# Performance work log

Measured on AMD Instinct MI355X. Metric: run time of the kernel, lower is better.

Reference implementation:

```python
import jax, jax.numpy as jnp
import numpy as np
from jax import lax

N = 16384; B = 8; L = N // B; E = 262144
UNI = 496; PE = 16; C = UNI + PE   # channels = 512 (num_heads_gnn=1 so hidden*heads == hidden)
S = 16; K = 4; DTR = 32            # mamba d_state=16, d_conv=4, dt_rank=ceil(512/16)=32


def _sinpe(pos, d):
    # matches sinusoidal_positional_embedding: emb[:,0::2]=sin(pos/denom), emb[:,1::2]=cos
    half = d // 2
    denom = jnp.power(10000.0, 2.0 * jnp.arange(half, dtype=pos.dtype) / d)
    ang = pos[:, None] / denom                       # [N, d//2]
    return jnp.stack([jnp.sin(ang), jnp.cos(ang)], axis=-1).reshape(pos.shape[0], d)


def _bn(h, g, b, eps=1e-5):
    # BatchNorm1d over node dim, batch statistics (training-style)
    mu = h.mean(0)
    var = jnp.mean((h - mu) ** 2, axis=0)
    return (h - mu) * lax.rsqrt(var + eps) * g + b


def setup_inputs() -> dict:
    key = jax.random.key(0)
    ks = jax.random.split(key, 48)
    r = lambda i, shape, s=0.02: jax.random.normal(ks[i], shape, jnp.float32) * s
    src = jax.random.randint(ks[0], (E,), 0, N, jnp.int32)
    off = jax.random.randint(ks[1], (E,), 1, N, jnp.int32)
    dst = (src + off) % N  # no self-loops: GATConv strips then re-adds them
    return dict(
        x=jax.random.normal(ks[2], (N, 1026), jnp.float32),
        edge_index=jnp.stack([src, dst]),
        edge_cat=jax.random.randint(ks[4], (E,), 0, 21, jnp.int32),
        edge_cont=jax.random.normal(ks[3], (E, 2), jnp.float32),
        batch=(jnp.arange(N, dtype=jnp.int32) // L),  # B contiguous equal-size graphs
        W_uni=r(5, (1024, UNI), 0.03), b_uni=r(6, (UNI,)),
        edge_emb=r(7, (21, 16), 1.0), W_edge=r(8, (2, 16), 0.5), b_edge=r(9, (16,)),
        W_gat=r(10, (C, C), 0.04), att_src=r(11, (C,), 0.06), att_dst=r(12, (C,), 0.06), b_gat=r(13, (C,)),
        g1=jnp.ones((C,), jnp.float32), be1=jnp.zeros((C,), jnp.float32),
        g2=jnp.ones((C,), jnp.float32), be2=jnp.zeros((C,), jnp.float32),
        g3=jnp.ones((C,), jnp.float32), be3=jnp.zeros((C,), jnp.float32),
        W_in=r(14, (C, 2 * C), 0.04), w_conv=r(15, (C, K), 0.3), b_conv=r(16, (C,)),
        W_xp=r(17, (C, DTR + 2 * S), 0.04), W_dt=r(18, (DTR, C), 0.1), b_dt=r(19, (C,), 0.5),
        A_log=jnp.log(jnp.tile(jnp.arange(1, S + 1, dtype=jnp.float32)[None, :], (C, 1))),
        D_p=jnp.ones((C,), jnp.float32), W_out=r(20, (C, C), 0.04),
        W_m1=r(21, (C, 2 * C), 0.04), b_m1=r(22, (2 * C,)),
        W_m2=r(23, (2 * C, C), 0.03), b_m2=r(24, (C,)),
        Wf1=r(25, (C, C // 2), 0.04), bf1=r(26, (C // 2,)),
        Wf2=r(27, (C // 2, C // 4), 0.06), bf2=r(28, (C // 4,)),
        Wf3=r(29, (C // 4, 1), 0.1), bf3=r(30, (1,)),
    )


def _forward(x, edge_cont, W_uni, b_uni, edge_emb, W_edge, b_edge, W_gat, att_src, att_dst,
             b_gat, g1, be1, g2, be2, g3, be3, W_in, w_conv, b_conv, W_xp, W_dt, b_dt,
             A_log, D_p, W_out, W_m1, b_m1, W_m2, b_m2, Wf1, bf1, Wf2, bf2, Wf3, bf3,
             edge_index, edge_cat, batch):
    # --- node features: UNI projection + 2D sinusoidal PE ---
    pe = jnp.concatenate([_sinpe(x[:, 0], PE // 2), _sinpe(x[:, 1], PE // 2)], axis=-1)  # [N,16]
    xf = x[:, 2:2 + 1024] @ W_uni + b_uni                                                # [N,496]
    h0 = jnp.concatenate([xf, pe], axis=-1)                                              # [N,512]
    # edge features are computed as in the original, but GATConv(edge_dim=None) ignores them
    _ef = edge_emb[edge_cat] + edge_cont @ W_edge + b_edge

    # --- GATConv, heads=1, concat, with self loops, eval (no dropout) ---
    xh = h0 @ W_gat                                  # [N,C]
    a_s = xh @ att_src                               # [N]
    a_d = xh @ att_dst
    loops = jnp.arange(N)
    src = jnp.concatenate([edge_index[0], loops])
    dst = jnp.concatenate([edge_index[1], loops])
    alpha = jax.nn.leaky_relu(a_s[src] + a_d[dst], 0.2)
    amax = jax.ops.segment_max(alpha, dst, num_segments=N)
    ea = jnp.exp(alpha - amax[dst])
    den = jax.ops.segment_sum(ea, dst, num_segments=N)
    w = ea / (den[dst] + 1e-16)
    gat = jax.ops.segment_sum(w[:, None] * xh[src], dst, num_segments=N) + b_gat
    h1 = _bn(gat, g1, be1)

    # --- Mamba branch on the LAYER INPUT h0; equal contiguous graphs -> reshape ---
    hd = h0.reshape(B, L, C)
    xz = hd @ W_in                                   # [B,L,2C]
    xm, z = xz[..., :C], xz[..., C:]
    xp = jnp.pad(xm, ((0, 0), (K - 1, 0), (0, 0)))   # causal depthwise conv, kernel K
    xc = b_conv + sum(xp[:, k:k + L, :] * w_conv[:, k] for k in range(K))
    xc = jax.nn.silu(xc)
    proj = xc @ W_xp                                 # [B,L,DTR+2S]
    dt = jax.nn.softplus(proj[..., :DTR] @ W_dt + b_dt)   # [B,L,C]
    Bm = proj[..., DTR:DTR + S]
    Cm = proj[..., DTR + S:]
    A = -jnp.exp(A_log)                              # [C,S]

    def step(hst, inp):
        xt, dtt, Bt, Ct = inp                        # [B,C],[B,C],[B,S],[B,S]
        hst = hst * jnp.exp(dtt[:, :, None] * A) + (dtt * xt)[:, :, None] * Bt[:, None, :]
        return hst, jnp.einsum('bds,bs->bd', hst, Ct)

    _, ys = lax.scan(step, jnp.zeros((B, C, S), hd.dtype),
                     (xc.swapaxes(0, 1), dt.swapaxes(0, 1), Bm.swapaxes(0, 1), Cm.swapaxes(0, 1)))
    y = ys.swapaxes(0, 1) + D_p * xc
    y = (y * jax.nn.silu(z)) @ W_out                 # [B,L,C]
    h2 = _bn(y.reshape(N, C), g2, be2)

    # --- combine, MLP residual, norm3, relu ---
    out = h1 + h2
    out = out + (jax.nn.relu(out @ W_m1 + b_m1) @ W_m2 + b_m2)
    out = jax.nn.relu(_bn(out, g3, be3))

    # --- global mean pool + head MLP ---
    pooled = out.reshape(B, L, C).mean(axis=1)       # [B,C]
    hm = jax.nn.relu(pooled @ Wf1 + bf1)
    hm = jax.nn.relu(hm @ Wf2 + bf2)
    pred = hm @ Wf3 + bf3                            # [B,1]
    return pred, pooled


def reference(x, edge_index, edge_cat, edge_cont, batch, W_uni, b_uni, edge_emb, W_edge,
              b_edge, W_gat, att_src, att_dst, b_gat, g1, be1, g2, be2, g3, be3, W_in,
              w_conv, b_conv, W_xp, W_dt, b_dt, A_log, D_p, W_out, W_m1, b_m1, W_m2, b_m2,
              Wf1, bf1, Wf2, bf2, Wf3, bf3):
    return _forward(x, edge_cont, W_uni, b_uni, edge_emb, W_edge, b_edge, W_gat, att_src,
                    att_dst, b_gat, g1, be1, g2, be2, g3, be3, W_in, w_conv, b_conv, W_xp,
                    W_dt, b_dt, A_log, D_p, W_out, W_m1, b_m1, W_m2, b_m2, Wf1, bf1, Wf2,
                    bf2, Wf3, bf3, edge_index, edge_cat, batch)
```

## Files before the change

### kernel.cpp

```cpp
#include <hip/hip_runtime.h>
#include <math.h>

#define NN 16384
#define CD 512
#define EE 262144
#define LL 2048
#define NCK 32
#define TC 64

typedef __attribute__((ext_vector_type(8))) short short8;
typedef __attribute__((ext_vector_type(4))) float floatx4;

__device__ __forceinline__ unsigned short f2b(float f){
  unsigned int u = __float_as_uint(f);
  unsigned int r = (u + 0x7fffu + ((u>>16)&1u)) >> 16;
  return (unsigned short)r;
}
__device__ __forceinline__ float b2f(unsigned short h){
  return __uint_as_float(((unsigned int)h)<<16);
}


__global__ void transposeW(const float* __restrict__ W, short* __restrict__ Bt,
                           int K, int Nsub, int Npad, int pitch, int col0){
  int idx = blockIdx.x*256 + threadIdx.x;
  if (idx >= Npad*K) return;
  int n = idx / K, k = idx - n*K;
  float v = (n < Nsub) ? W[(size_t)k*pitch + col0 + n] : 0.f;
  Bt[idx] = (short)f2b(v);
}

__global__ void fuse_wdt(const float* __restrict__ W_xp, const float* __restrict__ W_dt,
                         short* __restrict__ Wft){
  int idx = blockIdx.x*256 + threadIdx.x;
  if (idx >= 512*512) return;
  int i = idx & 511;
  int j = idx >> 9;
  float a = 0.f;
  #pragma unroll 8
  for (int r = 0; r < 32; ++r) a += W_xp[(size_t)i*64 + r] * W_dt[(size_t)r*512 + j];
  Wft[idx] = (short)f2b(a);
}

__global__ void pad_bias(const float* __restrict__ b, float* __restrict__ out){
  int i = blockIdx.x*256 + threadIdx.x;
  if (i < 512) out[i] = (i < 496) ? b[i] : 0.f;
}

__global__ void conv_x(const float* __restrict__ x, short* __restrict__ Xb){
  int idx = blockIdx.x*256 + threadIdx.x;
  if (idx >= NN*1024) return;
  int r = idx >> 10, c = idx & 1023;
  Xb[idx] = (short)f2b(x[(size_t)r*1026 + 2 + c]);
}

__global__ void pe_fill(const float* __restrict__ x, unsigned short* __restrict__ h0b){
  int r = blockIdx.x*256 + threadIdx.x;
  if (r >= NN) return;
  float p0 = x[(size_t)r*1026 + 0], p1 = x[(size_t)r*1026 + 1];
  const float dn[4] = {1.f, 10.f, 100.f, 1000.f};
  unsigned short* o = h0b + (size_t)r*512 + 496;
  #pragma unroll
  for (int q = 0; q < 4; ++q){
    o[2*q]     = f2b(sinf(p0/dn[q]));
    o[2*q+1]   = f2b(cosf(p0/dn[q]));
    o[8+2*q]   = f2b(sinf(p1/dn[q]));
    o[8+2*q+1] = f2b(cosf(p1/dn[q]));
  }
}

#define GLDS(g, l) __builtin_amdgcn_global_load_lds((const __attribute__((address_space(1))) void*)(g), (__attribute__((address_space(3))) void*)(l), 16, 0, 0)

__global__ __launch_bounds__(256)
void gemm_bt(const short* __restrict__ A, const short* __restrict__ Bt,
             float* __restrict__ Cf, unsigned short* __restrict__ Cb,
             const float* __restrict__ bias, const float* __restrict__ resid,
             int K, int Nvalid, int epi){
  __shared__ __align__(16) short As[128*32];
  __shared__ __align__(16) short Bs[128*32];
  int tid = threadIdx.x;
  int m0 = blockIdx.x * 128;
  int n0 = blockIdx.y * 128;
  int lane = tid & 63, wave = tid >> 6;
  int wm = wave >> 1, wn = wave & 1;
  int lr = lane & 15, lk = lane >> 4;

  floatx4 acc[4][4];
  #pragma unroll
  for (int m = 0; m < 4; ++m)
    #pragma unroll
    for (int n = 0; n < 4; ++n) acc[m][n] = (floatx4)0.f;

  int wrow = wave * 32;
  int srow = lane >> 2;
  int scol = (lane & 3) * 8;

  const short* gA0 = A  + (size_t)(m0 + wrow + srow)*K      + scol;
  const short* gA1 = A  + (size_t)(m0 + wrow + 16 + srow)*K + scol;
  const short* gB0 = Bt + (size_t)(n0 + wrow + srow)*K      + scol;
  const short* gB1 = Bt + (size_t)(n0 + wrow + 16 + srow)*K + scol;

  for (int k0 = 0; k0 < K; k0 += 32){
    __syncthreads();
    GLDS(gA0 + k0, &As[wrow*32]);
    GLDS(gA1 + k0, &As[(wrow+16)*32]);
    GLDS(gB0 + k0, &Bs[wrow*32]);
    GLDS(gB1 + k0, &Bs[(wrow+16)*32]);
    __syncthreads();
    short8 af[4], bf[4];
    #pragma unroll
    for (int m = 0; m < 4; ++m) af[m] = *(const short8*)&As[(wm*64 + m*16 + lr)*32 + lk*8];
    #pragma unroll
    for (int n = 0; n < 4; ++n) bf[n] = *(const short8*)&Bs[(wn*64 + n*16 + lr)*32 + lk*8];
    #pragma unroll
    for (int m = 0; m < 4; ++m)
      #pragma unroll
      for (int n = 0; n < 4; ++n)
        acc[m][n] = __builtin_amdgcn_mfma_f32_16x16x32_bf16(af[m], bf[n], acc[m][n], 0, 0, 0);
  }

  #pragma unroll
  for (int m = 0; m < 4; ++m){
    #pragma unroll
    for (int n = 0; n < 4; ++n){
      int col = n0 + wn*64 + n*16 + lr;
      if (col < Nvalid){
        #pragma unroll
        for (int r = 0; r < 4; ++r){
          int row = m0 + wm*64 + m*16 + lk*4 + r;
          float v = acc[m][n][r];
          if (bias)  v += bias[col];
          if (resid) v += resid[(size_t)row*Nvalid + col];
          if (epi == 1) v = fmaxf(v, 0.f);
          else if (epi == 2) v = (v > 20.f) ? v : log1pf(expf(v));
          size_t o = (size_t)row*Nvalid + col;
          if (Cf) Cf[o] = v;
          if (Cb) Cb[o] = f2b(v);
        }
      }
    }
  }
}

__global__ void att_proj(const unsigned short* __restrict__ xh,
                         const float* __restrict__ att_src, const float* __restrict__ att_dst,
                         float* __restrict__ a_s, float* __restrict__ a_d){
  int wave = threadIdx.x >> 6, lane = threadIdx.x & 63;
  int r = blockIdx.x*4 + wave;
  const unsigned short* xr = xh + (size_t)r*512;
  float ps = 0.f, pd = 0.f;
  #pragma unroll
  for (int j = 0; j < 8; ++j){
    float v = b2f(xr[lane + 64*j]);
    ps += v * att_src[lane + 64*j];
    pd += v * att_dst[lane + 64*j];
  }
  #pragma unroll
  for (int m = 32; m >= 1; m >>= 1){ ps += __shfl_xor(ps, m); pd += __shfl_xor(pd, m); }
  if (lane == 0){ a_s[r] = ps; a_d[r] = pd; }
}

__global__ void gat_hist(const int* __restrict__ ei, int* __restrict__ cnt){
  int e = blockIdx.x*256 + threadIdx.x;
  if (e < EE) atomicAdd(&cnt[ei[EE + e]], 1);
}

__global__ void gat_prefix(const int* __restrict__ cnt, int* __restrict__ offsets, int* __restrict__ cursor){
  __shared__ int part[256];
  int t = threadIdx.x;
  int s = 0;
  for (int i = 0; i < 64; ++i) s += cnt[t*64 + i];
  part[t] = s;
  __syncthreads();
  for (int off = 1; off < 256; off <<= 1){
    int v = (t >= off) ? part[t - off] : 0;
    __syncthreads();
    part[t] += v;
    __syncthreads();
  }
  int run = part[t] - s;
  for (int i = 0; i < 64; ++i){
    int c = cnt[t*64 + i];
    offsets[t*64 + i] = run;
    cursor[t*64 + i]  = run;
    run += c;
  }
  if (t == 255) offsets[NN] = run;
}

__global__ void gat_scatter(const int* __restrict__ ei, const float* __restrict__ a_s,
                            const float* __restrict__ a_d, int* __restrict__ cursor,
                            int* __restrict__ srcs, float* __restrict__ alphas){
  int e = blockIdx.x*256 + threadIdx.x;
  if (e >= EE) return;
  int sN = ei[e], dN = ei[EE + e];
  int p = atomicAdd(&cursor[dN], 1);
  srcs[p] = sN;
  float al = a_s[sN] + a_d[dN];
  alphas[p] = (al > 0.f) ? al : 0.2f*al;
}

__global__ __launch_bounds__(256)
void gat_agg(const int* __restrict__ offsets, const int* __restrict__ srcs,
             const float* __restrict__ alphas, const unsigned short* __restrict__ xh,
             const float* __restrict__ a_s, const float* __restrict__ a_d,
             const float* __restrict__ b_gat, float* __restrict__ gat){
  int wave = threadIdx.x >> 6, lane = threadIdx.x & 63;
  int i = blockIdx.x*4 + wave;
  int beg = offsets[i], end = offsets[i+1];
  float asd = a_s[i] + a_d[i];
  float al0 = (asd > 0.f) ? asd : 0.2f*asd;
  float mx = al0;
  for (int p = beg + lane; p < end; p += 64) mx = fmaxf(mx, alphas[p]);
  #pragma unroll
  for (int m = 32; m >= 1; m >>= 1) mx = fmaxf(mx, __shfl_xor(mx, m));
  float se = 0.f;
  for (int p = beg + lane; p < end; p += 64) se += expf(alphas[p] - mx);
  #pragma unroll
  for (int m = 32; m >= 1; m >>= 1) se += __shfl_xor(se, m);
  float den = se + expf(al0 - mx);
  float inv = 1.f/(den + 1e-16f);
  float acc[8] = {0,0,0,0,0,0,0,0};
  for (int p = beg; p < end; ++p){
    float w = expf(alphas[p] - mx) * inv;
    const unsigned short* xr = xh + (size_t)srcs[p]*512;
    #pragma unroll
    for (int j = 0; j < 8; ++j) acc[j] += w * b2f(xr[lane + 64*j]);
  }
  {
    float w0 = expf(al0 - mx) * inv;
    const unsigned short* xr = xh + (size_t)i*512;
    #pragma unroll
    for (int j = 0; j < 8; ++j) acc[j] += w0 * b2f(xr[lane + 64*j]);
  }
  #pragma unroll
  for (int j = 0; j < 8; ++j)
    gat[(size_t)i*512 + lane + 64*j] = acc[j] + b_gat[lane + 64*j];
}

__global__ void conv_silu(const unsigned short* __restrict__ xzb,
                          const float* __restrict__ w_conv, const float* __restrict__ b_conv,
                          float* __restrict__ xc, unsigned short* __restrict__ xcb){
  int r = blockIdx.x;
  int c = blockIdx.y*256 + threadIdx.x;
  int t = r & (LL - 1);
  float acc = b_conv[c];
  #pragma unroll
  for (int k = 0; k < 4; ++k){
    int tt = t + k - 3;
    if (tt >= 0) acc += b2f(xzb[(size_t)(r + k - 3)*1024 + c]) * w_conv[c*4 + k];
  }
  float s = acc / (1.f + expf(-acc));
  xc[(size_t)r*512 + c] = s;
  xcb[(size_t)r*512 + c] = f2b(s);
}

__global__ __launch_bounds__(256)
void ssm_scan1(const float* __restrict__ dt, const float* __restrict__ xc,
               const float* __restrict__ BC, const float* __restrict__ A_log,
               float* __restrict__ Pc, float* __restrict__ Hc){
  int s  = threadIdx.x & 15;
  int dl = threadIdx.x >> 4;
  int bc = blockIdx.x;
  int b  = bc >> 5;
  int ck = bc & (NCK - 1);
  int d  = blockIdx.y*16 + dl;
  float A = -expf(A_log[d*16 + s]);
  float h = 0.f, P = 1.f;
  size_t r = (size_t)b*LL + (size_t)ck*TC;
  for (int t = 0; t < TC; ++t, ++r){
    float dtv = dt[r*512 + d];
    float xv  = xc[r*512 + d];
    float Bv  = BC[r*32 + s];
    float a = expf(dtv * A);
    h = h*a + (dtv*xv)*Bv;
    P *= a;
  }
  size_t idx = ((size_t)bc*512 + d)*16 + s;
  Pc[idx] = P;
  Hc[idx] = h;
}

__global__ void ssm_carry(const float* __restrict__ Pc, float* __restrict__ Hc){
  int gid = blockIdx.x*256 + threadIdx.x;
  int b  = gid >> 13;
  int ds = gid & 8191;
  size_t idx = ((size_t)b*NCK)*8192 + ds;
  float carry = 0.f;
  for (int c = 0; c < NCK; ++c){
    float P = Pc[idx], H = Hc[idx];
    Hc[idx] = carry;
    carry = H + P*carry;
    idx += 8192;
  }
}

__global__ __launch_bounds__(256)
void ssm_scan2(const float* __restrict__ dt, const float* __restrict__ xc,
               const float* __restrict__ BC, const unsigned short* __restrict__ xzb,
               const float* __restrict__ A_log, const float* __restrict__ D_p,
               const float* __restrict__ Cin, unsigned short* __restrict__ yfb){
  int s  = threadIdx.x & 15;
  int dl = threadIdx.x >> 4;
  int bc = blockIdx.x;
  int b  = bc >> 5;
  int ck = bc & (NCK - 1);
  int d  = blockIdx.y*16 + dl;
  float A = -expf(A_log[d*16 + s]);
  float Dp = D_p[d];
  size_t idx = ((size_t)bc*512 + d)*16 + s;
  float h = Cin[idx];
  size_t r = (size_t)b*LL + (size_t)ck*TC;
  for (int t = 0; t < TC; ++t, ++r){
    float dtv = dt[r*512 + d];
    float xv  = xc[r*512 + d];
    float Bv  = BC[r*32 + s];
    float Cv  = BC[r*32 + 16 + s];
    float a = expf(dtv * A);
    h = h*a + (dtv*xv)*Bv;
    float y = h * Cv;
    y += __shfl_xor(y, 1);
    y += __shfl_xor(y, 2);
    y += __shfl_xor(y, 4);
    y += __shfl_xor(y, 8);
    if (s == 0){
      float z  = b2f(xzb[r*1024 + 512 + d]);
      float sz = z / (1.f + expf(-z));
      yfb[r*512 + d] = f2b((y + Dp*xv) * sz);
    }
  }
}

__global__ void colstats(const float* __restrict__ X, float* __restrict__ sums, float* __restrict__ sqs){
  int c0 = threadIdx.x;
  int row0 = blockIdx.x * 128;
  float s0=0,q0=0,s1=0,q1=0;
  for (int i = 0; i < 128; ++i){
    const float* rp = X + (size_t)(row0+i)*512;
    float a = rp[c0], b = rp[c0+256];
    s0 += a; q0 += a*a; s1 += b; q1 += b*b;
  }
  atomicAdd(&sums[c0], s0);      atomicAdd(&sqs[c0], q0);
  atomicAdd(&sums[c0+256], s1);  atomicAdd(&sqs[c0+256], q1);
}

__global__ void combine_out0(const float* __restrict__ gat, const float* __restrict__ h2,
                             const float* __restrict__ s1, const float* __restrict__ q1,
                             const float* __restrict__ s2, const float* __restrict__ q2,
                             const float* __restrict__ g1, const float* __restrict__ be1,
                             const float* __restrict__ g2, const float* __restrict__ be2,
                             float* __restrict__ out0, unsigned short* __restrict__ out0b){
  int t = threadIdx.x;
  int row0 = blockIdx.x * 128;
  const float invN = 1.f/16384.f;
  float sc1[2], sc2[2], off[2];
  #pragma unroll
  for (int h = 0; h < 2; ++h){
    int c = t + h*256;
    float m1 = s1[c]*invN, v1 = q1[c]*invN - m1*m1;
    float m2 = s2[c]*invN, v2 = q2[c]*invN - m2*m2;
    float a1 = rsqrtf(v1 + 1e-5f) * g1[c];
    float a2 = rsqrtf(v2 + 1e-5f) * g2[c];
    sc1[h] = a1; sc2[h] = a2;
    off[h] = be1[c] + be2[c] - m1*a1 - m2*a2;
  }
  for (int i = 0; i < 128; ++i){
    size_t ro = (size_t)(row0+i)*512;
    #pragma unroll
    for (int h = 0; h < 2; ++h){
      int c = t + h*256;
      float v = gat[ro+c]*sc1[h] + h2[ro+c]*sc2[h] + off[h];
      out0[ro+c] = v;
      out0b[ro+c] = f2b(v);
    }
  }
}

__global__ void out2_pool(const float* __restrict__ out1,
                          const float* __restrict__ s3, const float* __restrict__ q3,
                          const float* __restrict__ g3, const float* __restrict__ be3,
                          float* __restrict__ poolsum){
  int t = threadIdx.x;
  int row0 = blockIdx.x * 128;
  int bidx = row0 / LL;
  const float invN = 1.f/16384.f;
  float sc[2], off[2], acc[2] = {0.f, 0.f};
  #pragma unroll
  for (int h = 0; h < 2; ++h){
    int c = t + h*256;
    float m = s3[c]*invN, v = q3[c]*invN - m*m;
    float a = rsqrtf(v + 1e-5f) * g3[c];
    sc[h] = a; off[h] = be3[c] - m*a;
  }
  for (int i = 0; i < 128; ++i){
    size_t ro = (size_t)(row0+i)*512;
    #pragma unroll
    for (int h = 0; h < 2; ++h){
      int c = t + h*256;
      float v = fmaxf(out1[ro+c]*sc[h] + off[h], 0.f);
      acc[h] += v;
    }
  }
  atomicAdd(&poolsum[bidx*512 + t], acc[0]);
  atomicAdd(&poolsum[bidx*512 + t + 256], acc[1]);
}

__global__ __launch_bounds__(256)
void head(const float* __restrict__ poolsum,
          const float* __restrict__ Wf1, const float* __restrict__ bf1,
          const float* __restrict__ Wf2, const float* __restrict__ bf2,
          const float* __restrict__ Wf3, const float* __restrict__ bf3,
          float* __restrict__ dout){
  int r = blockIdx.x, t = threadIdx.x;
  __shared__ float pool[512];
  __shared__ float h1s[256];
  __shared__ float h2s[128];
  for (int i = t; i < 512; i += 256){
    float v = poolsum[r*512 + i] * (1.f/2048.f);
    pool[i] = v;
    dout[8 + r*512 + i] = v;
  }
  __syncthreads();
  {
    float a = bf1[t];
    for (int k = 0; k < 512; ++k) a += pool[k] * Wf1[(size_t)k*256 + t];
    h1s[t] = fmaxf(a, 0.f);
  }
  __syncthreads();
  if (t < 128){
    float a = bf2[t];
    for (int k = 0; k < 256; ++k) a += h1s[k] * Wf2[(size_t)k*128 + t];
    h2s[t] = fmaxf(a, 0.f);
  }
  __syncthreads();
  if (t == 0){
    float a = bf3[0];
    for (int k = 0; k < 128; ++k) a += h2s[k] * Wf3[k];
    dout[r] = a;
  }
}

extern "C" void kernel_launch(void* const* d_in, const int* in_sizes, int n_in,
                              void* d_out, int out_size, void* d_ws, size_t ws_size,
                              hipStream_t stream){
  const float* x      = (const float*)d_in[0];
  const int*   ei     = (const int*)d_in[1];
  const float* W_uni  = (const float*)d_in[5];
  const float* b_uni  = (const float*)d_in[6];
  const float* W_gat  = (const float*)d_in[10];
  const float* att_s  = (const float*)d_in[11];
  const float* att_d  = (const float*)d_in[12];
  const float* b_gat  = (const float*)d_in[13];
  const float* g1     = (const float*)d_in[14];
  const float* be1    = (const float*)d_in[15];
  const float* g2     = (const float*)d_in[16];
  const float* be2    = (const float*)d_in[17];
  const float* g3     = (const float*)d_in[18];
  const float* be3    = (const float*)d_in[19];
  const float* W_in   = (const float*)d_in[20];
  const float* w_conv = (const float*)d_in[21];
  const float* b_conv = (const float*)d_in[22];
  const float* W_xp   = (const float*)d_in[23];
  const float* W_dt   = (const float*)d_in[24];
  const float* b_dt   = (const float*)d_in[25];
  const float* A_log  = (const float*)d_in[26];
  const float* D_p    = (const float*)d_in[27];
  const float* W_out  = (const float*)d_in[28];
  const float* W_m1   = (const float*)d_in[29];
  const float* b_m1   = (const float*)d_in[30];
  const float* W_m2   = (const float*)d_in[31];
  const float* b_m2   = (const float*)d_in[32];
  const float* Wf1    = (const float*)d_in[33];
  const float* bf1    = (const float*)d_in[34];
  const float* Wf2    = (const float*)d_in[35];
  const float* bf2    = (const float*)d_in[36];
  const float* Wf3    = (const float*)d_in[37];
  const float* bf3    = (const float*)d_in[38];
  float* dout = (float*)d_out;

  char* base = (char*)d_ws;
  size_t off = 0;
  auto alloc = [&](size_t b){ size_t r = off; off += (b + 255) & ~(size_t)255; return r; };

  size_t oR1    = alloc((size_t)NN*1024*2);
  size_t oH0b   = alloc((size_t)NN*512*2);
  size_t oWuniT = alloc(512*1024*2);
  size_t oWgatT = alloc(512*512*2);
  size_t oWinT  = alloc(1024*512*2);
  size_t oWfusT = alloc(512*512*2);
  size_t oWbcT  = alloc(128*512*2);
  size_t oWoutT = alloc(512*512*2);
  size_t oWm1T  = alloc(1024*512*2);
  size_t oWm2T  = alloc(512*1024*2);
  size_t oBuni  = alloc(512*4);
  size_t oXh    = alloc((size_t)NN*512*2);
  size_t oAs    = alloc(NN*4);
  size_t oAd    = alloc(NN*4);
  size_t oCnt   = alloc(NN*4);
  size_t oCur   = alloc(NN*4);
  size_t oOff   = alloc((NN+1)*4);
  size_t oSrcs  = alloc((size_t)EE*4);
  size_t oAlph  = alloc((size_t)EE*4);
  size_t oGat   = alloc((size_t)NN*512*4);
  size_t oXc    = alloc((size_t)NN*512*4);
  size_t oXcb   = alloc((size_t)NN*512*2);
  size_t oDt    = alloc((size_t)NN*512*4);
  size_t oBC    = alloc((size_t)NN*32*4);
  size_t oStats = alloc(6*512*4);
  size_t oPool  = alloc(8*512*4);

  short* Xb   = (short*)(base + oR1);
  unsigned short* xzb = (unsigned short*)(base + oR1);
  float* out1 = (float*)(base + oR1);
  unsigned short* h0b = (unsigned short*)(base + oH0b);
  short* WuniT = (short*)(base + oWuniT);
  short* WgatT = (short*)(base + oWgatT);
  short* WinT  = (short*)(base + oWinT);
  short* WfusT = (short*)(base + oWfusT);
  short* WbcT  = (short*)(base + oWbcT);
  short* WoutT = (short*)(base + oWoutT);
  short* Wm1T  = (short*)(base + oWm1T);
  short* Wm2T  = (short*)(base + oWm2T);
  float* buniP = (float*)(base + oBuni);
  unsigned short* xh  = (unsigned short*)(base + oXh);
  unsigned short* yfb = (unsigned short*)(base + oXh);
  float* a_s = (float*)(base + oAs);
  float* a_d = (float*)(base + oAd);
  int* cnt = (int*)(base + oCnt);
  int* cur = (int*)(base + oCur);
  int* offs = (int*)(base + oOff);
  int* srcs = (int*)(base + oSrcs);
  float* alphas = (float*)(base + oAlph);
  float* gat = (float*)(base + oGat);
  unsigned short* mlp1b = (unsigned short*)(base + oGat);
  float* xc = (float*)(base + oXc);
  float* out0 = (float*)(base + oXc);
  unsigned short* xcb  = (unsigned short*)(base + oXcb);
  unsigned short* out0b = (unsigned short*)(base + oXcb);
  float* Pc = (float*)(base + oXcb);
  float* Hc = Pc + (size_t)8*NCK*512*16;
  float* dt = (float*)(base + oDt);
  float* h2raw = (float*)(base + oDt);
  float* BC = (float*)(base + oBC);
  float* s1 = (float*)(base + oStats);
  float* q1 = s1 + 512;
  float* s2 = q1 + 512;
  float* q2 = s2 + 512;
  float* s3 = q2 + 512;
  float* q3 = s3 + 512;
  float* poolsum = (float*)(base + oPool);

  hipMemsetAsync(cnt, 0, NN*4, stream);
  hipMemsetAsync(s1, 0, 6*512*4, stream);
  hipMemsetAsync(poolsum, 0, 8*512*4, stream);

  transposeW<<<(512*1024+255)/256, 256, 0, stream>>>(W_uni, WuniT, 1024, 496, 512, 496, 0);
  transposeW<<<(512*512+255)/256, 256, 0, stream>>>(W_gat, WgatT, 512, 512, 512, 512, 0);
  transposeW<<<(1024*512+255)/256, 256, 0, stream>>>(W_in, WinT, 512, 1024, 1024, 1024, 0);
  transposeW<<<(128*512+255)/256, 256, 0, stream>>>(W_xp, WbcT, 512, 32, 128, 64, 32);
  transposeW<<<(512*512+255)/256, 256, 0, stream>>>(W_out, WoutT, 512, 512, 512, 512, 0);
  transposeW<<<(1024*512+255)/256, 256, 0, stream>>>(W_m1, Wm1T, 512, 1024, 1024, 1024, 0);
  transposeW<<<(512*1024+255)/256, 256, 0, stream>>>(W_m2, Wm2T, 1024, 512, 512, 512, 0);
  fuse_wdt<<<(512*512+255)/256, 256, 0, stream>>>(W_xp, W_dt, WfusT);
  pad_bias<<<2, 256, 0, stream>>>(b_uni, buniP);
  conv_x<<<(NN*1024+255)/256, 256, 0, stream>>>(x, Xb);

  dim3 g4(128, 4), g8(128, 8), g1b(128, 1);
  gemm_bt<<<g4, 256, 0, stream>>>(Xb, WuniT, nullptr, h0b, buniP, nullptr, 1024, 512, 0);
  pe_fill<<<(NN+255)/256, 256, 0, stream>>>(x, h0b);
  gemm_bt<<<g4, 256, 0, stream>>>((const short*)h0b, WgatT, nullptr, xh, nullptr, nullptr, 512, 512, 0);
  att_proj<<<NN/4, 256, 0, stream>>>(xh, att_s, att_d, a_s, a_d);
  gat_hist<<<EE/256, 256, 0, stream>>>(ei, cnt);
  gat_prefix<<<1, 256, 0, stream>>>(cnt, offs, cur);
  gat_scatter<<<EE/256, 256, 0, stream>>>(ei, a_s, a_d, cur, srcs, alphas);
  gat_agg<<<NN/4, 256, 0, stream>>>(offs, srcs, alphas, xh, a_s, a_d, b_gat, gat);
  colstats<<<128, 256, 0, stream>>>(gat, s1, q1);
  gemm_bt<<<g8, 256, 0, stream>>>((const short*)h0b, WinT, nullptr, xzb, nullptr, nullptr, 512, 1024, 0);
  {
    dim3 gc(NN, 2);
    conv_silu<<<gc, 256, 0, stream>>>(xzb, w_conv, b_conv, xc, xcb);
  }
  gemm_bt<<<g4, 256, 0, stream>>>((const short*)xcb, WfusT, dt, nullptr, b_dt, nullptr, 512, 512, 2);
  gemm_bt<<<g1b, 256, 0, stream>>>((const short*)xcb, WbcT, BC, nullptr, nullptr, nullptr, 512, 32, 0);
  {
    dim3 gs(8*NCK, 32);
    ssm_scan1<<<gs, 256, 0, stream>>>(dt, xc, BC, A_log, Pc, Hc);
    ssm_carry<<<256, 256, 0, stream>>>(Pc, Hc);
    ssm_scan2<<<gs, 256, 0, stream>>>(dt, xc, BC, xzb, A_log, D_p, Hc, yfb);
  }
  gemm_bt<<<g4, 256, 0, stream>>>((const short*)yfb, WoutT, h2raw, nullptr, nullptr, nullptr, 512, 512, 0);
  colstats<<<128, 256, 0, stream>>>(h2raw, s2, q2);
  combine_out0<<<128, 256, 0, stream>>>(gat, h2raw, s1, q1, s2, q2, g1, be1, g2, be2, out0, out0b);
  gemm_bt<<<g8, 256, 0, stream>>>((const short*)out0b, Wm1T, nullptr, mlp1b, b_m1, nullptr, 512, 1024, 1);
  gemm_bt<<<g4, 256, 0, stream>>>((const short*)mlp1b, Wm2T, out1, nullptr, b_m2, out0, 1024, 512, 0);
  colstats<<<128, 256, 0, stream>>>(out1, s3, q3);
  out2_pool<<<128, 256, 0, stream>>>(out1, s3, q3, g3, be3, poolsum);
  head<<<8, 256, 0, stream>>>(poolsum, Wf1, bf1, Wf2, bf2, Wf3, bf3, dout);
}
```

Measured before the change: 1.117 ms.

## Restructure SSM scan to one thread per channel holding all 16 states

The selective-scan kernels now give each thread one channel and keep all 16 state values in registers, instead of one thread per (channel, state) pair. dt and x are loaded once per channel rather than 16 times, B and C are read as vector loads, and the cross-lane shuffle reduction for y is removed. The chunk decay product is computed in closed form as exp(A·sum(dt)). Fast __expf replaces expf in the GAT aggregation, conv SiLU and scan kernels. The scan grids shrink from 32 to 2 y-blocks, which lowers parallelism and raises register pressure, and the fast exp and closed-form product may change rounding slightly.

Measured after the change: 915.2 us. -18.1%, faster.

```diff
diff --git a/kernel.cpp b/kernel.cpp
--- a/kernel.cpp
+++ b/kernel.cpp
@@ -215,20 +215,20 @@
   #pragma unroll
   for (int m = 32; m >= 1; m >>= 1) mx = fmaxf(mx, __shfl_xor(mx, m));
   float se = 0.f;
-  for (int p = beg + lane; p < end; p += 64) se += expf(alphas[p] - mx);
+  for (int p = beg + lane; p < end; p += 64) se += __expf(alphas[p] - mx);
   #pragma unroll
   for (int m = 32; m >= 1; m >>= 1) se += __shfl_xor(se, m);
-  float den = se + expf(al0 - mx);
+  float den = se + __expf(al0 - mx);
   float inv = 1.f/(den + 1e-16f);
   float acc[8] = {0,0,0,0,0,0,0,0};
   for (int p = beg; p < end; ++p){
-    float w = expf(alphas[p] - mx) * inv;
+    float w = __expf(alphas[p] - mx) * inv;
     const unsigned short* xr = xh + (size_t)srcs[p]*512;
     #pragma unroll
     for (int j = 0; j < 8; ++j) acc[j] += w * b2f(xr[lane + 64*j]);
   }
   {
-    float w0 = expf(al0 - mx) * inv;
+    float w0 = __expf(al0 - mx) * inv;
     const unsigned short* xr = xh + (size_t)i*512;
     #pragma unroll
     for (int j = 0; j < 8; ++j) acc[j] += w0 * b2f(xr[lane + 64*j]);
@@ -250,7 +250,7 @@
     int tt = t + k - 3;
     if (tt >= 0) acc += b2f(xzb[(size_t)(r + k - 3)*1024 + c]) * w_conv[c*4 + k];
   }
-  float s = acc / (1.f + expf(-acc));
+  float s = acc / (1.f + __expf(-acc));
   xc[(size_t)r*512 + c] = s;
   xcb[(size_t)r*512 + c] = f2b(s);
 }
@@ -259,26 +259,41 @@
 void ssm_scan1(const float* __restrict__ dt, const float* __restrict__ xc,
                const float* __restrict__ BC, const float* __restrict__ A_log,
                float* __restrict__ Pc, float* __restrict__ Hc){
-  int s  = threadIdx.x & 15;
-  int dl = threadIdx.x >> 4;
+  int d  = blockIdx.y*256 + threadIdx.x;
   int bc = blockIdx.x;
   int b  = bc >> 5;
   int ck = bc & (NCK - 1);
-  int d  = blockIdx.y*16 + dl;
-  float A = -expf(A_log[d*16 + s]);
-  float h = 0.f, P = 1.f;
+  float A[16], h[16];
+  #pragma unroll
+  for (int s = 0; s < 16; ++s){ A[s] = -__expf(A_log[d*16 + s]); h[s] = 0.f; }
+  float sdt = 0.f;
   size_t r = (size_t)b*LL + (size_t)ck*TC;
   for (int t = 0; t < TC; ++t, ++r){
     float dtv = dt[r*512 + d];
     float xv  = xc[r*512 + d];
-    float Bv  = BC[r*32 + s];
-    float a = expf(dtv * A);
-    h = h*a + (dtv*xv)*Bv;
-    P *= a;
-  }
-  size_t idx = ((size_t)bc*512 + d)*16 + s;
-  Pc[idx] = P;
-  Hc[idx] = h;
+    float dx  = dtv * xv;
+    const floatx4* bp = (const floatx4*)&BC[r*32];
+    float Bf[16];
+    *(floatx4*)&Bf[0]  = bp[0];
+    *(floatx4*)&Bf[4]  = bp[1];
+    *(floatx4*)&Bf[8]  = bp[2];
+    *(floatx4*)&Bf[12] = bp[3];
+    #pragma unroll
+    for (int s = 0; s < 16; ++s){
+      float a = __expf(dtv * A[s]);
+      h[s] = h[s]*a + dx*Bf[s];
+    }
+    sdt += dtv;
+  }
+  size_t idx = ((size_t)bc*512 + d)*16;
+  float P[16];
+  #pragma unroll
+  for (int s = 0; s < 16; ++s) P[s] = __expf(A[s]*sdt);
+  #pragma unroll
+  for (int q = 0; q < 4; ++q){
+    *(floatx4*)&Pc[idx + q*4] = *(floatx4*)&P[q*4];
+    *(floatx4*)&Hc[idx + q*4] = *(floatx4*)&h[q*4];
+  }
 }
 
 __global__ void ssm_carry(const float* __restrict__ Pc, float* __restrict__ Hc){
@@ -300,34 +315,40 @@
                const float* __restrict__ BC, const unsigned short* __restrict__ xzb,
                const float* __restrict__ A_log, const float* __restrict__ D_p,
                const float* __restrict__ Cin, unsigned short* __restrict__ yfb){
-  int s  = threadIdx.x & 15;
-  int dl = threadIdx.x >> 4;
+  int d  = blockIdx.y*256 + threadIdx.x;
   int bc = blockIdx.x;
   int b  = bc >> 5;
   int ck = bc & (NCK - 1);
-  int d  = blockIdx.y*16 + dl;
-  float A = -expf(A_log[d*16 + s]);
+  float A[16], h[16];
+  size_t idx = ((size_t)bc*512 + d)*16;
+  #pragma unroll
+  for (int s = 0; s < 16; ++s){ A[s] = -__expf(A_log[d*16 + s]); h[s] = Cin[idx + s]; }
   float Dp = D_p[d];
-  size_t idx = ((size_t)bc*512 + d)*16 + s;
-  float h = Cin[idx];
   size_t r = (size_t)b*LL + (size_t)ck*TC;
   for (int t = 0; t < TC; ++t, ++r){
     float dtv = dt[r*512 + d];
     float xv  = xc[r*512 + d];
-    float Bv  = BC[r*32 + s];
-    float Cv  = BC[r*32 + 16 + s];
-    float a = expf(dtv * A);
-    h = h*a + (dtv*xv)*Bv;
-    float y = h * Cv;
-    y += __shfl_xor(y, 1);
-    y += __shfl_xor(y, 2);
-    y += __shfl_xor(y, 4);
-    y += __shfl_xor(y, 8);
-    if (s == 0){
-      float z  = b2f(xzb[r*1024 + 512 + d]);
-      float sz = z / (1.f + expf(-z));
-      yfb[r*512 + d] = f2b((y + Dp*xv) * sz);
+    float dx  = dtv * xv;
+    const floatx4* bp = (const floatx4*)&BC[r*32];
+    float Bf[16], Cf[16];
+    *(floatx4*)&Bf[0]  = bp[0];
+    *(floatx4*)&Bf[4]  = bp[1];
+    *(floatx4*)&Bf[8]  = bp[2];
+    *(floatx4*)&Bf[12] = bp[3];
+    *(floatx4*)&Cf[0]  = bp[4];
+    *(floatx4*)&Cf[4]  = bp[5];
+    *(floatx4*)&Cf[8]  = bp[6];
+    *(floatx4*)&Cf[12] = bp[7];
+    float y = 0.f;
+    #pragma unroll
+    for (int s = 0; s < 16; ++s){
+      float a = __expf(dtv * A[s]);
+      h[s] = h[s]*a + dx*Bf[s];
+      y += h[s]*Cf[s];
     }
+    float z  = b2f(xzb[r*1024 + 512 + d]);
+    float sz = z / (1.f + __expf(-z));
+    yfb[r*512 + d] = f2b((y + Dp*xv) * sz);
   }
 }
 
@@ -583,7 +604,7 @@
   gemm_bt<<<g4, 256, 0, stream>>>((const short*)xcb, WfusT, dt, nullptr, b_dt, nullptr, 512, 512, 2);
   gemm_bt<<<g1b, 256, 0, stream>>>((const short*)xcb, WbcT, BC, nullptr, nullptr, nullptr, 512, 32, 0);
   {
-    dim3 gs(8*NCK, 32);
+    dim3 gs(8*NCK, 2);
     ssm_scan1<<<gs, 256, 0, stream>>>(dt, xc, BC, A_log, Pc, Hc);
     ssm_carry<<<256, 256, 0, stream>>>(Pc, Hc);
     ssm_scan2<<<gs, 256, 0, stream>>>(dt, xc, BC, xzb, A_log, D_p, Hc, yfb);
```
